# Performance work log

Measured on AMD Instinct MI355X. Metric: run time of the kernel, lower is better.

## Reference

```python
import jax, jax.numpy as jnp
import numpy as np

# SLAYER neuron / simulation hyperparameters (from network.yaml)
THETA = 10.0      # spike threshold
TAU_SR = 10.0     # SRM (PSP) kernel time constant [ms]
TAU_REF = 1.0     # refractory kernel time constant [ms]
SCALE_REF = 2.0   # refractory kernel scale
TS = 1.0          # simulation step [ms]
K_SRM = 100       # truncation length of SRM kernel (eps decays ~0 by 10*tau)
K_REF = 32        # truncation length of refractory kernel (tauRef=1 -> decays fast)


def _eps_kernel(tau, k):
    # eps(t) = (t/tau) * exp(1 - t/tau), eps(0) = 0  (SLAYER SRM alpha kernel)
    t = jnp.arange(k, dtype=jnp.float32) * TS
    return (t / tau) * jnp.exp(1.0 - t / tau)


def psp(x, kern):
    # Causal temporal filter: y[..., t] = sum_j kern[j] * x[..., t - j]
    B, N, T = x.shape
    lhs = x.reshape(B * N, 1, T)
    rhs = kern[::-1].reshape(1, 1, -1)  # lax.conv is cross-correlation -> flip
    y = jax.lax.conv_general_dilated(
        lhs, rhs, window_strides=(1,), padding=[(kern.shape[0] - 1, 0)],
        dimension_numbers=('NCH', 'OIH', 'NCH'))
    return y.reshape(B, N, T)


def spike(u, refk):
    # Sequential thresholding with refractory feedback (SLAYER spikeFunction fwd).
    # u: [B, N, T] membrane drive. State r: future refractory contributions.
    kr = refk.shape[0]
    refk_shift = jnp.concatenate([refk[1:], jnp.zeros((1,), refk.dtype)])

    def step(r, u_t):
        m = u_t + r[..., 0]                      # membrane potential at t
        s = (m >= THETA).astype(u_t.dtype)       # hard spike
        r_next = jnp.concatenate([r[..., 1:], jnp.zeros_like(r[..., :1])], -1) \
                 + s[..., None] * refk_shift     # add refractory response
        return r_next, s

    uT = jnp.moveaxis(u, -1, 0)                  # [T, B, N]
    r0 = jnp.zeros(uT.shape[1:] + (kr,), u.dtype)
    _, sT = jax.lax.scan(step, r0, uT)
    return jnp.moveaxis(sT, 0, -1) / TS          # [B, N, T]


def setup_inputs() -> dict:
    key = jax.random.key(0)
    k1, k2, k3 = jax.random.split(key, 3)
    B, NIN, NHID, NOUT, T = 32, 2048, 512, 10, 350
    spike_input = (jax.random.uniform(k1, (B, NIN, T)) < 0.05).astype(jnp.float32)
    W1 = jax.random.normal(k2, (NHID, NIN), dtype=jnp.float32) * 0.05
    W2 = jax.random.normal(k3, (NOUT, NHID), dtype=jnp.float32) * 0.05
    return {"spike_input": spike_input, "W1": W1, "W2": W2}


def reference(spike_input, W1, W2):
    srm = _eps_kernel(TAU_SR, K_SRM)
    refk = -SCALE_REF * THETA * _eps_kernel(TAU_REF, K_REF)
    # layer 1: psp -> dense -> spike
    a1 = jnp.einsum('bnt,mn->bmt', psp(spike_input, srm), W1)
    s1 = spike(a1, refk)
    # layer 2: psp -> dense -> spike
    a2 = jnp.einsum('bnt,mn->bmt', psp(s1, srm), W2)
    s2 = spike(a2, refk)
    return s2
```

## Files before the change

kernel.cpp:

```cpp
#include <hip/hip_runtime.h>
#include <stdint.h>

static constexpr int B  = 32;
static constexpr int T  = 350;
static constexpr int NIN = 2048;
static constexpr int NH  = 512;
static constexpr int NO  = 10;
static constexpr int BT  = B * T;

static constexpr float THETA = 10.0f;
static constexpr float BETA  = 0.36787944117144233f;
static constexpr float CREF  = 54.365636569180904707f;

static constexpr size_t OFF_W1T  = 0;
static constexpr size_t OFF_MASK = 4196352;
static constexpr size_t OFF_SRM  = 7063552;
static constexpr size_t OFF_Z1   = 7064576;
static constexpr size_t OFF_A1   = 30002176;
static constexpr size_t OFF_Z2   = OFF_Z1;

__global__ void __launch_bounds__(256) k_prep(const float* __restrict__ x,
                                              const float* __restrict__ W1,
                                              float* __restrict__ W1T,
                                              uint64_t* __restrict__ mask,
                                              float* __restrict__ srm28) {
    int bid = blockIdx.x;
    if (bid < 1024) {
        __shared__ uint64_t tb[6][64];
        int b = bid >> 5, nblk = bid & 31;
        int wv = threadIdx.x >> 6, lane = threadIdx.x & 63;
        for (int g = 0; g < 4; ++g) {
            float v[4][6];
            #pragma unroll
            for (int i = 0; i < 4; ++i) {
                int nr = wv + 4 * (4 * g + i);
                const float* xp = x + ((size_t)b * NIN + nblk * 64 + nr) * T;
                #pragma unroll
                for (int c = 0; c < 6; ++c) {
                    int t = c * 64 + lane;
                    v[i][c] = (t < T) ? xp[t] : 0.f;
                }
            }
            #pragma unroll
            for (int i = 0; i < 4; ++i) {
                int nr = wv + 4 * (4 * g + i);
                #pragma unroll
                for (int c = 0; c < 6; ++c) {
                    uint64_t mk = __ballot(v[i][c] != 0.0f);
                    if (lane == 0) tb[c][nr] = mk;
                }
            }
        }
        __syncthreads();
        static const uint64_t AM[6] = {
            0x00000000FFFFFFFFull, 0x0000FFFF0000FFFFull, 0x00FF00FF00FF00FFull,
            0x0F0F0F0F0F0F0F0Full, 0x3333333333333333ull, 0x5555555555555555ull };
        for (int c = wv; c < 6; c += 4) {
            uint64_t w = tb[c][lane];
            #pragma unroll
            for (int i = 0; i < 6; ++i) {
                int s = 32 >> i;
                uint64_t A = AM[i];
                uint64_t y = __shfl_xor((unsigned long long)w, s);
                if ((lane & s) == 0) w = (w & A)  | ((y & A) << s);
                else                 w = (w & ~A) | ((y & ~A) >> s);
            }
            int t = c * 64 + lane;
            if (t < T) mask[((size_t)b * T + t) * 32 + nblk] = w;
        }
    } else if (bid < 2048) {
        __shared__ float tile[32][33];
        int idx = bid - 1024;
        int n0 = (idx & 63) * 32, m0 = (idx >> 6) * 32;
        int tx = threadIdx.x & 31, ty0 = threadIdx.x >> 5;
        #pragma unroll
        for (int i = 0; i < 4; ++i) {
            int ty = ty0 + 8 * i;
            tile[ty][tx] = W1[(size_t)(m0 + ty) * NIN + n0 + tx];
        }
        __syncthreads();
        #pragma unroll
        for (int i = 0; i < 4; ++i) {
            int ty = ty0 + 8 * i;
            W1T[(size_t)(n0 + ty) * NH + m0 + tx] = tile[tx][ty];
        }
    } else {
        int j = threadIdx.x;
        if (j < 192) {
            float v = 0.f;
            int i = j - 28;
            if (i >= 0 && i < 100) { float t = (float)i; v = (t * 0.1f) * expf(1.f - t * 0.1f); }
            srm28[j] = v;
        }
        for (int i = j; i < NH; i += 256) W1T[(size_t)2048 * NH + i] = 0.f;
    }
}

__global__ void __launch_bounds__(64) k_z1(const uint64_t* __restrict__ mask,
                                           const float* __restrict__ W1T,
                                           float* __restrict__ z1) {
    __shared__ alignas(8) uint16_t lst[288];
    int row = blockIdx.x, lane = threadIdx.x;
    const uint64_t* mrow = mask + (size_t)row * 32;
    uint64_t w = (lane < 32) ? mrow[lane] : 0ull;
    int cnt = __popcll(w);
    int pre = cnt;
    #pragma unroll
    for (int off = 1; off < 64; off <<= 1) {
        int v = __shfl_up(pre, off);
        if (lane >= off) pre += v;
    }
    int total = __shfl(pre, 63);
    int excl = pre - cnt;
    while (w) {
        int bit = __builtin_ctzll(w);
        w &= w - 1;
        lst[excl++] = (uint16_t)((lane << 6) + bit);
    }
    int padded = (total + 3) & ~3;
    if (lane < padded - total) lst[total + lane] = 2048;
    __syncthreads();

    const float4* W4 = (const float4*)W1T;
    float4 a0 = {0,0,0,0}, a1v = {0,0,0,0};
    int i0 = lane * 2, i1 = lane * 2 + 1;
    for (int k = 0; k < padded; k += 4) {
        ushort4 q = *(const ushort4*)(lst + k);
        const float4* p0 = W4 + (size_t)q.x * 128;
        const float4* p1 = W4 + (size_t)q.y * 128;
        const float4* p2 = W4 + (size_t)q.z * 128;
        const float4* p3 = W4 + (size_t)q.w * 128;
        float4 x0 = p0[i0], y0 = p0[i1];
        float4 x1 = p1[i0], y1 = p1[i1];
        float4 x2 = p2[i0], y2 = p2[i1];
        float4 x3 = p3[i0], y3 = p3[i1];
        a0.x += x0.x; a0.y += x0.y; a0.z += x0.z; a0.w += x0.w;
        a1v.x += y0.x; a1v.y += y0.y; a1v.z += y0.z; a1v.w += y0.w;
        a0.x += x1.x; a0.y += x1.y; a0.z += x1.z; a0.w += x1.w;
        a1v.x += y1.x; a1v.y += y1.y; a1v.z += y1.z; a1v.w += y1.w;
        a0.x += x2.x; a0.y += x2.y; a0.z += x2.z; a0.w += x2.w;
        a1v.x += y2.x; a1v.y += y2.y; a1v.z += y2.z; a1v.w += y2.w;
        a0.x += x3.x; a0.y += x3.y; a0.z += x3.z; a0.w += x3.w;
        a1v.x += y3.x; a1v.y += y3.y; a1v.z += y3.z; a1v.w += y3.w;
    }
    float4* zp = (float4*)(z1 + (size_t)row * NH);
    zp[i0] = a0; zp[i1] = a1v;
}

__global__ void __launch_bounds__(64) k_fir1(const float* __restrict__ src,
                                             float* __restrict__ dst,
                                             const float* __restrict__ srm28) {
    __shared__ float tb[192];
    int b = blockIdx.x, half = blockIdx.y, tg = blockIdx.z;
    int lane = threadIdx.x;
    for (int i = lane; i < 192; i += 64) tb[i] = srm28[i];
    __syncthreads();
    int t0 = tg * 16;
    int m = half * 256 + lane * 4;
    const float* sp = src + (size_t)b * T * NH + m;

    float4 acc[16];
    #pragma unroll
    for (int r = 0; r < 16; ++r) acc[r] = make_float4(0.f, 0.f, 0.f, 0.f);
    float c[16];
    #pragma unroll
    for (int r = 0; r < 16; ++r) c[r] = tb[r + 127];

    for (int o = 0; o < 8; ++o) {
        #pragma unroll
        for (int j = 0; j < 16; ++j) {
            int dd = o * 16 + j;
            int tau = t0 - 99 + dd;
            float4 v = make_float4(0.f, 0.f, 0.f, 0.f);
            if (tau >= 0 && tau < T) v = *(const float4*)(sp + (size_t)tau * NH);
            #pragma unroll
            for (int r = 0; r < 16; ++r) {
                acc[r].x += c[r] * v.x; acc[r].y += c[r] * v.y;
                acc[r].z += c[r] * v.z; acc[r].w += c[r] * v.w;
            }
            #pragma unroll
            for (int r = 15; r > 0; --r) c[r] = c[r - 1];
            int ci = 126 - dd;
            c[0] = tb[ci < 0 ? 0 : ci];
        }
    }
    #pragma unroll
    for (int r = 0; r < 16; ++r) {
        int t = t0 + r;
        if (t < T) *(float4*)(dst + ((size_t)b * T + t) * NH + m) = acc[r];
    }
}

__global__ void __launch_bounds__(512) k_scanz2(const float* __restrict__ a1,
                                                const float* __restrict__ W2,
                                                float* __restrict__ z2) {
    __shared__ float w2s[NO * NH];
    __shared__ uint64_t smask[16][8];
    constexpr int CT = 16;
    constexpr int NC = (T + CT - 1) / CT;
    int b = blockIdx.x, tid = threadIdx.x;
    int wv = tid >> 6;
    for (int i = tid; i < NO * NH; i += 512) w2s[i] = W2[i];
    const float* up = a1 + (size_t)b * T * NH + tid;
    float A = 0.f, Bs = 0.f;
    float cur[CT], nxt[CT];
    #pragma unroll
    for (int j = 0; j < CT; ++j) cur[j] = up[(size_t)j * NH];
    __syncthreads();
    for (int c = 0; c < NC; ++c) {
        int t0 = c * CT;
        int nsteps = (T - t0 < CT) ? (T - t0) : CT;
        if (c + 1 < NC) {
            #pragma unroll
            for (int j = 0; j < CT; ++j) {
                int t = t0 + CT + j;
                nxt[j] = (t < T) ? up[(size_t)t * NH] : 0.f;
            }
        }
        #pragma unroll
        for (int j = 0; j < CT; ++j) {
            if (j < nsteps) {
                float mem = cur[j] - CREF * Bs;
                float sp = (mem >= THETA) ? 1.0f : 0.0f;
                A = sp + BETA * A;
                Bs = BETA * (Bs + A);
                uint64_t mk = __ballot(sp != 0.0f);
                if ((tid & 63) == 0) smask[j][wv] = mk;
            }
        }
        __syncthreads();
        if (tid < nsteps * NO) {
            int j = tid / NO, o = tid - j * NO;
            const float* wrow = w2s + o * NH;
            float acc = 0.f;
            #pragma unroll
            for (int w8 = 0; w8 < 8; ++w8) {
                uint64_t mk = smask[j][w8];
                int base = w8 * 64;
                while (mk) {
                    int bit = __builtin_ctzll(mk);
                    mk &= mk - 1;
                    acc += wrow[base + bit];
                }
            }
            z2[((size_t)b * T + t0 + j) * NO + o] = acc;
        }
        __syncthreads();
        #pragma unroll
        for (int j = 0; j < CT; ++j) cur[j] = nxt[j];
    }
}

__global__ void __launch_bounds__(256) k_fir2scan(const float* __restrict__ z2,
                                                  const float* __restrict__ srm28,
                                                  float* __restrict__ out) {
    __shared__ float tb[192];
    __shared__ float zb[350 * 11 + 16];
    __shared__ float ab[352 * 10];
    int b = blockIdx.x, tid = threadIdx.x;
    if (tid < 192) tb[tid] = srm28[tid];
    const float* zp = z2 + (size_t)b * T * NO;
    for (int i = tid; i < T * NO; i += 256) {
        int t = i / NO, o = i - t * NO;
        zb[t * 11 + o] = zp[i];
    }
    __syncthreads();
    if (tid < 220) {
        int tt = tid / 10, o = tid - tt * 10;
        int t0 = tt * 16;
        float acc[16];
        #pragma unroll
        for (int r = 0; r < 16; ++r) acc[r] = 0.f;
        float c[16];
        #pragma unroll
        for (int r = 0; r < 16; ++r) c[r] = tb[r + 127];
        for (int oo = 0; oo < 8; ++oo) {
            #pragma unroll
            for (int j = 0; j < 16; ++j) {
                int dd = oo * 16 + j;
                int tau = t0 - 99 + dd;
                float v = (tau >= 0 && tau < T) ? zb[tau * 11 + o] : 0.f;
                #pragma unroll
                for (int r = 0; r < 16; ++r) acc[r] += c[r] * v;
                #pragma unroll
                for (int r = 15; r > 0; --r) c[r] = c[r - 1];
                int ci = 126 - dd;
                c[0] = tb[ci < 0 ? 0 : ci];
            }
        }
        #pragma unroll
        for (int r = 0; r < 16; ++r) {
            int t = t0 + r;
            if (t < T) ab[t * 10 + o] = acc[r];
        }
    }
    __syncthreads();
    if (tid < NO) {
        int o = tid;
        float A = 0.f, Bs = 0.f;
        float* op = out + ((size_t)b * NO + o) * T;
        for (int t = 0; t < T; ++t) {
            float mem = ab[t * 10 + o] - CREF * Bs;
            float sp = (mem >= THETA) ? 1.0f : 0.0f;
            A = sp + BETA * A;
            Bs = BETA * (Bs + A);
            op[t] = sp;
        }
    }
}

extern "C" void kernel_launch(void* const* d_in, const int* in_sizes, int n_in,
                              void* d_out, int out_size, void* d_ws, size_t ws_size,
                              hipStream_t stream) {
    const float* x  = (const float*)d_in[0];
    const float* W1 = (const float*)d_in[1];
    const float* W2 = (const float*)d_in[2];
    char* ws = (char*)d_ws;
    float*    W1T  = (float*)(ws + OFF_W1T);
    uint64_t* mask = (uint64_t*)(ws + OFF_MASK);
    float*    srm  = (float*)(ws + OFF_SRM);
    float*    z1   = (float*)(ws + OFF_Z1);
    float*    a1   = (float*)(ws + OFF_A1);
    float*    z2   = (float*)(ws + OFF_Z2);
    float*    out  = (float*)d_out;

    hipLaunchKernelGGL(k_prep,     dim3(2049),     dim3(256), 0, stream, x, W1, W1T, mask, srm);
    hipLaunchKernelGGL(k_z1,       dim3(BT),       dim3(64),  0, stream, mask, W1T, z1);
    hipLaunchKernelGGL(k_fir1,     dim3(B, 2, 22), dim3(64),  0, stream, z1, a1, srm);
    hipLaunchKernelGGL(k_scanz2,   dim3(B),        dim3(512), 0, stream, a1, W2, z2);
    hipLaunchKernelGGL(k_fir2scan, dim3(B),        dim3(256), 0, stream, z2, srm, out);
}
```

Baseline: 323.2 us.

## Split sparse gather into decode pass and two column-half gather passes

Spike-mask decoding moves into its own kernel that writes per-row index lists and counts to global memory, and the mask layout is transposed so each t is read contiguously per n-block. The gather-accumulate then runs as two separate launches, each covering half of the 512 output columns with one float4 per lane, unrolled by 8 indices. Splitting by column half is meant to shrink the active W1T working set per launch so more of it stays in L2/MALL, and the deeper unroll adds memory-level parallelism. The cost is an extra global write and read of the index lists, reading them twice, and two additional kernel launches.

```diff
diff --git a/kernel.cpp b/kernel.cpp
--- a/kernel.cpp
+++ b/kernel.cpp
@@ -14,9 +14,11 @@
 
 static constexpr size_t OFF_W1T  = 0;
 static constexpr size_t OFF_MASK = 4196352;
-static constexpr size_t OFF_SRM  = 7063552;
-static constexpr size_t OFF_Z1   = 7064576;
-static constexpr size_t OFF_A1   = 30002176;
+static constexpr size_t OFF_SRM  = 7080960;
+static constexpr size_t OFF_Z1   = 7081984;
+static constexpr size_t OFF_A1   = 30019584;
+static constexpr size_t OFF_LST  = OFF_A1;
+static constexpr size_t OFF_CNT  = OFF_A1 + 4300800;
 static constexpr size_t OFF_Z2   = OFF_Z1;
 
 __global__ void __launch_bounds__(256) k_prep(const float* __restrict__ x,
@@ -66,7 +68,7 @@
                 else                 w = (w & ~A) | ((y & ~A) >> s);
             }
             int t = c * 64 + lane;
-            if (t < T) mask[((size_t)b * T + t) * 32 + nblk] = w;
+            if (t < T) mask[((size_t)b * 32 + nblk) * 352 + t] = w;
         }
     } else if (bid < 2048) {
         __shared__ float tile[32][33];
@@ -96,13 +98,14 @@
     }
 }
 
-__global__ void __launch_bounds__(64) k_z1(const uint64_t* __restrict__ mask,
-                                           const float* __restrict__ W1T,
-                                           float* __restrict__ z1) {
-    __shared__ alignas(8) uint16_t lst[288];
-    int row = blockIdx.x, lane = threadIdx.x;
-    const uint64_t* mrow = mask + (size_t)row * 32;
-    uint64_t w = (lane < 32) ? mrow[lane] : 0ull;
+__global__ void __launch_bounds__(64) k_decode(const uint64_t* __restrict__ mask,
+                                               uint16_t* __restrict__ glst,
+                                               int* __restrict__ gcnt) {
+    __shared__ uint16_t lst[192];
+    int t = blockIdx.x, b = blockIdx.y;
+    int row = b * T + t;
+    int lane = threadIdx.x;
+    uint64_t w = (lane < 32) ? mask[((size_t)b * 32 + lane) * 352 + t] : 0ull;
     int cnt = __popcll(w);
     int pre = cnt;
     #pragma unroll
@@ -117,34 +120,46 @@
         w &= w - 1;
         lst[excl++] = (uint16_t)((lane << 6) + bit);
     }
-    int padded = (total + 3) & ~3;
+    int padded = (total + 7) & ~7;
     if (lane < padded - total) lst[total + lane] = 2048;
     __syncthreads();
-
+    uint16_t* op = glst + (size_t)row * 192;
+    for (int i = lane; i < padded; i += 64) op[i] = lst[i];
+    if (lane == 0) gcnt[row] = padded;
+}
+
+template<int H>
+__global__ void __launch_bounds__(64) k_z1g(const uint16_t* __restrict__ glst,
+                                            const int* __restrict__ gcnt,
+                                            const float* __restrict__ W1T,
+                                            float* __restrict__ z1) {
+    int row = blockIdx.x, lane = threadIdx.x;
+    int padded = gcnt[row];
+    const ushort4* lp = (const ushort4*)(glst + (size_t)row * 192);
     const float4* W4 = (const float4*)W1T;
-    float4 a0 = {0,0,0,0}, a1v = {0,0,0,0};
-    int i0 = lane * 2, i1 = lane * 2 + 1;
-    for (int k = 0; k < padded; k += 4) {
-        ushort4 q = *(const ushort4*)(lst + k);
-        const float4* p0 = W4 + (size_t)q.x * 128;
-        const float4* p1 = W4 + (size_t)q.y * 128;
-        const float4* p2 = W4 + (size_t)q.z * 128;
-        const float4* p3 = W4 + (size_t)q.w * 128;
-        float4 x0 = p0[i0], y0 = p0[i1];
-        float4 x1 = p1[i0], y1 = p1[i1];
-        float4 x2 = p2[i0], y2 = p2[i1];
-        float4 x3 = p3[i0], y3 = p3[i1];
-        a0.x += x0.x; a0.y += x0.y; a0.z += x0.z; a0.w += x0.w;
-        a1v.x += y0.x; a1v.y += y0.y; a1v.z += y0.z; a1v.w += y0.w;
-        a0.x += x1.x; a0.y += x1.y; a0.z += x1.z; a0.w += x1.w;
-        a1v.x += y1.x; a1v.y += y1.y; a1v.z += y1.z; a1v.w += y1.w;
-        a0.x += x2.x; a0.y += x2.y; a0.z += x2.z; a0.w += x2.w;
-        a1v.x += y2.x; a1v.y += y2.y; a1v.z += y2.z; a1v.w += y2.w;
-        a0.x += x3.x; a0.y += x3.y; a0.z += x3.z; a0.w += x3.w;
-        a1v.x += y3.x; a1v.y += y3.y; a1v.z += y3.z; a1v.w += y3.w;
-    }
-    float4* zp = (float4*)(z1 + (size_t)row * NH);
-    zp[i0] = a0; zp[i1] = a1v;
+    float4 acc = {0, 0, 0, 0};
+    int idx = H * 64 + lane;
+    for (int k = 0; k < padded; k += 8) {
+        ushort4 q0 = lp[k >> 2];
+        ushort4 q1 = lp[(k >> 2) + 1];
+        float4 x0 = W4[(size_t)q0.x * 128 + idx];
+        float4 x1 = W4[(size_t)q0.y * 128 + idx];
+        float4 x2 = W4[(size_t)q0.z * 128 + idx];
+        float4 x3 = W4[(size_t)q0.w * 128 + idx];
+        float4 x4 = W4[(size_t)q1.x * 128 + idx];
+        float4 x5 = W4[(size_t)q1.y * 128 + idx];
+        float4 x6 = W4[(size_t)q1.z * 128 + idx];
+        float4 x7 = W4[(size_t)q1.w * 128 + idx];
+        acc.x += x0.x; acc.y += x0.y; acc.z += x0.z; acc.w += x0.w;
+        acc.x += x1.x; acc.y += x1.y; acc.z += x1.z; acc.w += x1.w;
+        acc.x += x2.x; acc.y += x2.y; acc.z += x2.z; acc.w += x2.w;
+        acc.x += x3.x; acc.y += x3.y; acc.z += x3.z; acc.w += x3.w;
+        acc.x += x4.x; acc.y += x4.y; acc.z += x4.z; acc.w += x4.w;
+        acc.x += x5.x; acc.y += x5.y; acc.z += x5.z; acc.w += x5.w;
+        acc.x += x6.x; acc.y += x6.y; acc.z += x6.z; acc.w += x6.w;
+        acc.x += x7.x; acc.y += x7.y; acc.z += x7.z; acc.w += x7.w;
+    }
+    ((float4*)(z1 + (size_t)row * NH))[idx] = acc;
 }
 
 __global__ void __launch_bounds__(64) k_fir1(const float* __restrict__ src,
@@ -321,12 +336,16 @@
     float*    srm  = (float*)(ws + OFF_SRM);
     float*    z1   = (float*)(ws + OFF_Z1);
     float*    a1   = (float*)(ws + OFF_A1);
+    uint16_t* glst = (uint16_t*)(ws + OFF_LST);
+    int*      gcnt = (int*)(ws + OFF_CNT);
     float*    z2   = (float*)(ws + OFF_Z2);
     float*    out  = (float*)d_out;
 
-    hipLaunchKernelGGL(k_prep,     dim3(2049),     dim3(256), 0, stream, x, W1, W1T, mask, srm);
-    hipLaunchKernelGGL(k_z1,       dim3(BT),       dim3(64),  0, stream, mask, W1T, z1);
-    hipLaunchKernelGGL(k_fir1,     dim3(B, 2, 22), dim3(64),  0, stream, z1, a1, srm);
-    hipLaunchKernelGGL(k_scanz2,   dim3(B),        dim3(512), 0, stream, a1, W2, z2);
-    hipLaunchKernelGGL(k_fir2scan, dim3(B),        dim3(256), 0, stream, z2, srm, out);
-}
+    hipLaunchKernelGGL(k_prep,       dim3(2049),     dim3(256), 0, stream, x, W1, W1T, mask, srm);
+    hipLaunchKernelGGL(k_decode,     dim3(T, B),     dim3(64),  0, stream, mask, glst, gcnt);
+    hipLaunchKernelGGL((k_z1g<0>),   dim3(BT),       dim3(64),  0, stream, glst, gcnt, W1T, z1);
+    hipLaunchKernelGGL((k_z1g<1>),   dim3(BT),       dim3(64),  0, stream, glst, gcnt, W1T, z1);
+    hipLaunchKernelGGL(k_fir1,       dim3(B, 2, 22), dim3(64),  0, stream, z1, a1, srm);
+    hipLaunchKernelGGL(k_scanz2,     dim3(B),        dim3(512), 0, stream, a1, W2, z2);
+    hipLaunchKernelGGL(k_fir2scan,   dim3(B),        dim3(256), 0, stream, z2, srm, out);
+}
```

Result: no change. 327.7 us (+1.4%).
